# Kernel optimization log

Measured on AMD Instinct MI355X. Metric: run time of the kernel, lower is better.

The kernel has to match this reference:

```python
import jax, jax.numpy as jnp
import numpy as np

B, D, C = 4096, 4096, 1024


def setup_inputs() -> dict:
    key = jax.random.key(0)
    kx, kw = jax.random.split(key)
    x = jax.random.normal(kx, (B, D), dtype=jnp.float32)
    # kaiming_normal_ with nonlinearity='relu': std = sqrt(2 / fan_in)
    W = jax.random.normal(kw, (C, D), dtype=jnp.float32) * jnp.sqrt(2.0 / D)
    return {"x": x, "W": W}


def reference(x, W):
    # Original: -( (x[:, :, None] - W.T[None, :, :])**2 ).mean(axis=1)
    d = x.shape[1]
    x_sq = jnp.sum(x * x, axis=1, keepdims=True)        # [B, 1]
    w_sq = jnp.sum(W * W, axis=1)[None, :]              # [1, C]
    cross = jnp.einsum('bd,cd->bc', x, W)               # [B, C] tensor-core GEMM
    return -(x_sq - 2.0 * cross + w_sq) / d
```

## Files before the change

### kernel.cpp

```cpp
#include <hip/hip_runtime.h>
#include <hip/hip_bf16.h>


typedef float f32x4 __attribute__((ext_vector_type(4)));
typedef unsigned short ushort4_t __attribute__((ext_vector_type(4)));
typedef long long2_t __attribute__((ext_vector_type(2)));

#define BDIM 4096
#define DDIM 4096
#define CDIM 1024
#define TM 128
#define TN 128
#define BK 64
#define KSPLIT 4
#define NIT ((DDIM / KSPLIT) / BK)
#define SCALE 32.0f
#define INV_SS (1.0f/1024.0f)

__device__ __forceinline__ unsigned short f2bf(float f) {
    unsigned int u = __float_as_uint(f);
    unsigned int rounding = 0x7FFFu + ((u >> 16) & 1u);
    return (unsigned short)((u + rounding) >> 16);
}

__global__ __launch_bounds__(256) void cvt_rowsq(
    const float* __restrict__ x, const float* __restrict__ W,
    unsigned char* __restrict__ xb, unsigned char* __restrict__ wb,
    float* __restrict__ xsq, float* __restrict__ wsq)
{
    const int lane = threadIdx.x & 63;
    const int row = blockIdx.x * 4 + (threadIdx.x >> 6);

    const float* src;
    unsigned char* dst;
    float* sq;
    if (row < BDIM) {
        src = x + (size_t)row * DDIM;
        dst = xb + (size_t)row * DDIM;
        sq = xsq + row;
    } else {
        int r = row - BDIM;
        src = W + (size_t)r * DDIM;
        dst = wb + (size_t)r * DDIM;
        sq = wsq + r;
    }

    const float4* s4 = (const float4*)src;
    unsigned int* d4 = (unsigned int*)dst;
    float a = 0.f;
    #pragma unroll
    for (int s = 0; s < DDIM / 4 / 64; ++s) {
        float4 f = s4[lane + 64 * s];
        a += f.x * f.x + f.y * f.y + f.z * f.z + f.w * f.w;
        unsigned int p = 0;
        p = __builtin_amdgcn_cvt_pk_fp8_f32(f.x * SCALE, f.y * SCALE, p, false);
        p = __builtin_amdgcn_cvt_pk_fp8_f32(f.z * SCALE, f.w * SCALE, p, true);
        d4[lane + 64 * s] = p;
    }
    #pragma unroll
    for (int off = 32; off > 0; off >>= 1) a += __shfl_down(a, off);
    if (lane == 0) *sq = a;
}

__global__ __launch_bounds__(256, 3) void gemm_eucl(
    const unsigned char* __restrict__ xb,
    const unsigned char* __restrict__ wb,
    unsigned short* __restrict__ part)
{
    __shared__ unsigned char sm[2 * 16384];

    const int tid = threadIdx.x;
    const int lane = tid & 63;
    const int wid = tid >> 6;
    const int bm = blockIdx.x * TM;
    const int bn = blockIdx.y * TN;
    const int ks = blockIdx.z * (DDIM / KSPLIT);
    const int wm = (wid >> 1) * 64;
    const int wn = (wid & 1) * 64;

    const int r0 = tid >> 2, c = tid & 3;
    const unsigned char* gA0 = xb + (size_t)(bm + r0) * DDIM + ks + c * 16;
    const unsigned char* gA1 = gA0 + (size_t)64 * DDIM;
    const unsigned char* gB0 = wb + (size_t)(bn + r0) * DDIM + ks + c * 16;
    const unsigned char* gB1 = gB0 + (size_t)64 * DDIM;

    const int k2o = (c >> 1) * 8;
    const int kcw = (c & 1) * 2;
    const int wo0 = r0 * 64 + ((kcw ^ (r0 & 3)) * 16) + k2o;
    const int wo1 = r0 * 64 + (((kcw | 1) ^ (r0 & 3)) * 16) + k2o;

    const int kc = lane >> 4;
    const int ml = lane & 15;
    int aoff[4], boff[4];
    #pragma unroll
    for (int i = 0; i < 4; ++i) {
        int m = wm + i * 16 + ml;
        aoff[i] = m * 64 + ((kc ^ (m & 3)) * 16);
        int n = wn + i * 16 + ml;
        boff[i] = n * 64 + ((kc ^ (n & 3)) * 16);
    }

    f32x4 acc[4][4] = {};
    long2_t pA0, pA1, pB0, pB1;

    pA0 = *(const long2_t*)gA0; pA1 = *(const long2_t*)gA1;
    pB0 = *(const long2_t*)gB0; pB1 = *(const long2_t*)gB1;
    gA0 += BK; gA1 += BK; gB0 += BK; gB1 += BK;
    {
        unsigned char* sA = sm;
        unsigned char* sB = sm + 8192;
        *(long*)(sA + wo0) = pA0.x; *(long*)(sA + wo1) = pA0.y;
        *(long*)(sA + wo0 + 4096) = pA1.x; *(long*)(sA + wo1 + 4096) = pA1.y;
        *(long*)(sB + wo0) = pB0.x; *(long*)(sB + wo1) = pB0.y;
        *(long*)(sB + wo0 + 4096) = pB1.x; *(long*)(sB + wo1 + 4096) = pB1.y;
    }
    __syncthreads();

    int pb = 0;
    for (int k = 0; k < NIT - 1; ++k) {
        pA0 = *(const long2_t*)gA0; pA1 = *(const long2_t*)gA1;
        pB0 = *(const long2_t*)gB0; pB1 = *(const long2_t*)gB1;
        gA0 += BK; gA1 += BK; gB0 += BK; gB1 += BK;

        {
            const unsigned char* sA = sm + pb * 16384;
            const unsigned char* sB = sA + 8192;
            long2_t la[4], lb[4];
            #pragma unroll
            for (int i = 0; i < 4; ++i) la[i] = *(const long2_t*)(sA + aoff[i]);
            #pragma unroll
            for (int j = 0; j < 4; ++j) lb[j] = *(const long2_t*)(sB + boff[j]);
            #pragma unroll
            for (int i = 0; i < 4; ++i)
                #pragma unroll
                for (int j = 0; j < 4; ++j) {
                    acc[i][j] = __builtin_amdgcn_mfma_f32_16x16x32_fp8_fp8(
                        la[i].x, lb[j].x, acc[i][j], 0, 0, 0);
                    acc[i][j] = __builtin_amdgcn_mfma_f32_16x16x32_fp8_fp8(
                        la[i].y, lb[j].y, acc[i][j], 0, 0, 0);
                }
        }

        {
            unsigned char* sA = sm + (pb ^ 1) * 16384;
            unsigned char* sB = sA + 8192;
            *(long*)(sA + wo0) = pA0.x; *(long*)(sA + wo1) = pA0.y;
            *(long*)(sA + wo0 + 4096) = pA1.x; *(long*)(sA + wo1 + 4096) = pA1.y;
            *(long*)(sB + wo0) = pB0.x; *(long*)(sB + wo1) = pB0.y;
            *(long*)(sB + wo0 + 4096) = pB1.x; *(long*)(sB + wo1 + 4096) = pB1.y;
        }
        __syncthreads();
        pb ^= 1;
    }

    {
        const unsigned char* sA = sm + pb * 16384;
        const unsigned char* sB = sA + 8192;
        long2_t la[4], lb[4];
        #pragma unroll
        for (int i = 0; i < 4; ++i) la[i] = *(const long2_t*)(sA + aoff[i]);
        #pragma unroll
        for (int j = 0; j < 4; ++j) lb[j] = *(const long2_t*)(sB + boff[j]);
        #pragma unroll
        for (int i = 0; i < 4; ++i)
            #pragma unroll
            for (int j = 0; j < 4; ++j) {
                acc[i][j] = __builtin_amdgcn_mfma_f32_16x16x32_fp8_fp8(
                    la[i].x, lb[j].x, acc[i][j], 0, 0, 0);
                acc[i][j] = __builtin_amdgcn_mfma_f32_16x16x32_fp8_fp8(
                    la[i].y, lb[j].y, acc[i][j], 0, 0, 0);
            }
    }

    unsigned short* p = part + (size_t)blockIdx.z * BDIM * CDIM
                      + (size_t)(blockIdx.x * 8 + blockIdx.y) * 16384;
    #pragma unroll
    for (int i = 0; i < 4; ++i)
        #pragma unroll
        for (int j = 0; j < 4; ++j) {
            ushort4_t v;
            v[0] = f2bf(acc[i][j][0]); v[1] = f2bf(acc[i][j][1]);
            v[2] = f2bf(acc[i][j][2]); v[3] = f2bf(acc[i][j][3]);
            *(ushort4_t*)&p[(i * 4 + j) * 1024 + tid * 4] = v;
        }
}

__global__ __launch_bounds__(256) void reduce_out(
    const unsigned short* __restrict__ part, const float* __restrict__ xsq,
    const float* __restrict__ wsq, float* __restrict__ out)
{
    const int bb = blockIdx.x;
    const int t = threadIdx.x;
    const int lane = t & 63;
    const int wid = t >> 6;
    const int bm = (bb >> 3) * TM, bn = (bb & 7) * TN;
    const int wm = (wid >> 1) * 64, wn = (wid & 1) * 64;
    const int row_l = (lane >> 4) * 4, col_l = lane & 15;
    const size_t sl = (size_t)BDIM * CDIM;
    const float c1 = 2.0f * INV_SS / (float)DDIM;
    const float c2 = 1.0f / (float)DDIM;

    #pragma unroll
    for (int f = 0; f < 16; ++f) {
        size_t o = (size_t)bb * 16384 + f * 1024 + t * 4;
        ushort4_t p0 = *(const ushort4_t*)&part[o];
        ushort4_t p1 = *(const ushort4_t*)&part[o + sl];
        ushort4_t p2 = *(const ushort4_t*)&part[o + 2 * sl];
        ushort4_t p3 = *(const ushort4_t*)&part[o + 3 * sl];
        int i = f >> 2, j = f & 3;
        int gn = bn + wn + j * 16 + col_l;
        float wv = wsq[gn];
        #pragma unroll
        for (int r = 0; r < 4; ++r) {
            float s = __uint_as_float((unsigned int)p0[r] << 16)
                    + __uint_as_float((unsigned int)p1[r] << 16)
                    + __uint_as_float((unsigned int)p2[r] << 16)
                    + __uint_as_float((unsigned int)p3[r] << 16);
            int gm = bm + wm + i * 16 + row_l + r;
            out[(size_t)gm * CDIM + gn] = s * c1 - (xsq[gm] + wv) * c2;
        }
    }
}

__global__ void fallback_kernel(const float* __restrict__ x, const float* __restrict__ W,
                                float* __restrict__ out)
{
    int c = blockIdx.x * blockDim.x + threadIdx.x;
    int b = blockIdx.y;
    if (c >= CDIM) return;
    const float* xr = x + (size_t)b * DDIM;
    const float* wr = W + (size_t)c * DDIM;
    float xs = 0.f, ws = 0.f, cr = 0.f;
    for (int d = 0; d < DDIM; ++d) {
        float xv = xr[d], wv = wr[d];
        xs += xv * xv; ws += wv * wv; cr += xv * wv;
    }
    out[(size_t)b * CDIM + c] = (2.0f * cr - xs - ws) / (float)DDIM;
}

extern "C" void kernel_launch(void* const* d_in, const int* in_sizes, int n_in,
                              void* d_out, int out_size, void* d_ws, size_t ws_size,
                              hipStream_t stream) {
    const float* x = (const float*)d_in[0];
    const float* W = (const float*)d_in[1];
    float* out = (float*)d_out;

    size_t need = (size_t)(BDIM + CDIM) * DDIM
                + (size_t)(BDIM + CDIM) * sizeof(float)
                + (size_t)KSPLIT * BDIM * CDIM * 2;
    if (ws_size < need) {
        fallback_kernel<<<dim3(CDIM / 256, BDIM), 256, 0, stream>>>(x, W, out);
        return;
    }

    unsigned char* xb = (unsigned char*)d_ws;
    unsigned char* wb = xb + (size_t)BDIM * DDIM;
    float* xsq = (float*)(wb + (size_t)CDIM * DDIM);
    float* wsq = xsq + BDIM;
    unsigned short* part = (unsigned short*)(wsq + CDIM);

    cvt_rowsq<<<(BDIM + CDIM) / 4, 256, 0, stream>>>(x, W, xb, wb, xsq, wsq);
    gemm_eucl<<<dim3(BDIM / TM, CDIM / TN, KSPLIT), 256, 0, stream>>>(xb, wb, part);
    reduce_out<<<256, 256, 0, stream>>>(part, xsq, wsq, out);
}
```

Measured before the change: 149.9 us.

## Deepen global prefetch to two register sets and use an LDS-only barrier

The GEMM main loop now keeps two sets of global-load registers in flight, unrolled by two with explicit LDS buffer indices. It also swaps __syncthreads for an inline s_waitcnt lgkmcnt(0) plus s_barrier, so outstanding global loads no longer have to drain at every barrier. The goal is to hide more global-memory latency behind the MFMA work. The cost is extra VGPRs per thread, which could hurt occupancy under the 3-blocks-per-CU launch bound, and correctness now depends on the compiler placing vmcnt waits before the LDS writes.

```diff
diff --git a/kernel.cpp b/kernel.cpp
--- a/kernel.cpp
+++ b/kernel.cpp
@@ -16,6 +16,8 @@
 #define NIT ((DDIM / KSPLIT) / BK)
 #define SCALE 32.0f
 #define INV_SS (1.0f/1024.0f)
+
+#define SYNC_LGKM() asm volatile("s_waitcnt lgkmcnt(0)\n\ts_barrier" ::: "memory")
 
 __device__ __forceinline__ unsigned short f2bf(float f) {
     unsigned int u = __float_as_uint(f);
@@ -62,6 +64,8 @@
     if (lane == 0) *sq = a;
 }
 
+struct Pref { long2_t a0, a1, b0, b1; };
+
 __global__ __launch_bounds__(256, 3) void gemm_eucl(
     const unsigned char* __restrict__ xb,
     const unsigned char* __restrict__ wb,
@@ -101,76 +105,67 @@
     }
 
     f32x4 acc[4][4] = {};
-    long2_t pA0, pA1, pB0, pB1;
-
-    pA0 = *(const long2_t*)gA0; pA1 = *(const long2_t*)gA1;
-    pB0 = *(const long2_t*)gB0; pB1 = *(const long2_t*)gB1;
-    gA0 += BK; gA1 += BK; gB0 += BK; gB1 += BK;
-    {
-        unsigned char* sA = sm;
-        unsigned char* sB = sm + 8192;
-        *(long*)(sA + wo0) = pA0.x; *(long*)(sA + wo1) = pA0.y;
-        *(long*)(sA + wo0 + 4096) = pA1.x; *(long*)(sA + wo1 + 4096) = pA1.y;
-        *(long*)(sB + wo0) = pB0.x; *(long*)(sB + wo1) = pB0.y;
-        *(long*)(sB + wo0 + 4096) = pB1.x; *(long*)(sB + wo1 + 4096) = pB1.y;
-    }
-    __syncthreads();
-
-    int pb = 0;
-    for (int k = 0; k < NIT - 1; ++k) {
-        pA0 = *(const long2_t*)gA0; pA1 = *(const long2_t*)gA1;
-        pB0 = *(const long2_t*)gB0; pB1 = *(const long2_t*)gB1;
-        gA0 += BK; gA1 += BK; gB0 += BK; gB1 += BK;
-
-        {
-            const unsigned char* sA = sm + pb * 16384;
-            const unsigned char* sB = sA + 8192;
-            long2_t la[4], lb[4];
-            #pragma unroll
-            for (int i = 0; i < 4; ++i) la[i] = *(const long2_t*)(sA + aoff[i]);
-            #pragma unroll
-            for (int j = 0; j < 4; ++j) lb[j] = *(const long2_t*)(sB + boff[j]);
-            #pragma unroll
-            for (int i = 0; i < 4; ++i)
-                #pragma unroll
-                for (int j = 0; j < 4; ++j) {
-                    acc[i][j] = __builtin_amdgcn_mfma_f32_16x16x32_fp8_fp8(
-                        la[i].x, lb[j].x, acc[i][j], 0, 0, 0);
-                    acc[i][j] = __builtin_amdgcn_mfma_f32_16x16x32_fp8_fp8(
-                        la[i].y, lb[j].y, acc[i][j], 0, 0, 0);
-                }
-        }
-
-        {
-            unsigned char* sA = sm + (pb ^ 1) * 16384;
-            unsigned char* sB = sA + 8192;
-            *(long*)(sA + wo0) = pA0.x; *(long*)(sA + wo1) = pA0.y;
-            *(long*)(sA + wo0 + 4096) = pA1.x; *(long*)(sA + wo1 + 4096) = pA1.y;
-            *(long*)(sB + wo0) = pB0.x; *(long*)(sB + wo1) = pB0.y;
-            *(long*)(sB + wo0 + 4096) = pB1.x; *(long*)(sB + wo1 + 4096) = pB1.y;
-        }
-        __syncthreads();
-        pb ^= 1;
-    }
-
-    {
-        const unsigned char* sA = sm + pb * 16384;
-        const unsigned char* sB = sA + 8192;
-        long2_t la[4], lb[4];
-        #pragma unroll
-        for (int i = 0; i < 4; ++i) la[i] = *(const long2_t*)(sA + aoff[i]);
-        #pragma unroll
-        for (int j = 0; j < 4; ++j) lb[j] = *(const long2_t*)(sB + boff[j]);
-        #pragma unroll
-        for (int i = 0; i < 4; ++i)
-            #pragma unroll
-            for (int j = 0; j < 4; ++j) {
-                acc[i][j] = __builtin_amdgcn_mfma_f32_16x16x32_fp8_fp8(
-                    la[i].x, lb[j].x, acc[i][j], 0, 0, 0);
-                acc[i][j] = __builtin_amdgcn_mfma_f32_16x16x32_fp8_fp8(
-                    la[i].y, lb[j].y, acc[i][j], 0, 0, 0);
-            }
-    }
+
+#define LOADSET(S)                                                      \
+    do {                                                                \
+        (S).a0 = *(const long2_t*)gA0; (S).a1 = *(const long2_t*)gA1;   \
+        (S).b0 = *(const long2_t*)gB0; (S).b1 = *(const long2_t*)gB1;   \
+        gA0 += BK; gA1 += BK; gB0 += BK; gB1 += BK;                     \
+    } while (0)
+
+#define WRITESET(buf, S)                                                \
+    do {                                                                \
+        unsigned char* sA = sm + (buf) * 16384;                         \
+        unsigned char* sB = sA + 8192;                                  \
+        *(long*)(sA + wo0) = (S).a0.x; *(long*)(sA + wo1) = (S).a0.y;   \
+        *(long*)(sA + wo0 + 4096) = (S).a1.x;                           \
+        *(long*)(sA + wo1 + 4096) = (S).a1.y;                           \
+        *(long*)(sB + wo0) = (S).b0.x; *(long*)(sB + wo1) = (S).b0.y;   \
+        *(long*)(sB + wo0 + 4096) = (S).b1.x;                           \
+        *(long*)(sB + wo1 + 4096) = (S).b1.y;                           \
+    } while (0)
+
+#define COMPUTE(buf)                                                    \
+    do {                                                                \
+        const unsigned char* sA = sm + (buf) * 16384;                   \
+        const unsigned char* sB = sA + 8192;                            \
+        long2_t la[4], lb[4];                                           \
+        _Pragma("unroll")                                               \
+        for (int i = 0; i < 4; ++i) la[i] = *(const long2_t*)(sA + aoff[i]); \
+        _Pragma("unroll")                                               \
+        for (int j = 0; j < 4; ++j) lb[j] = *(const long2_t*)(sB + boff[j]); \
+        _Pragma("unroll")                                               \
+        for (int i = 0; i < 4; ++i)                                     \
+            _Pragma("unroll")                                           \
+            for (int j = 0; j < 4; ++j) {                               \
+                acc[i][j] = __builtin_amdgcn_mfma_f32_16x16x32_fp8_fp8( \
+                    la[i].x, lb[j].x, acc[i][j], 0, 0, 0);              \
+                acc[i][j] = __builtin_amdgcn_mfma_f32_16x16x32_fp8_fp8( \
+                    la[i].y, lb[j].y, acc[i][j], 0, 0, 0);              \
+            }                                                           \
+    } while (0)
+
+    Pref S0, S1;
+    LOADSET(S0);
+    LOADSET(S1);
+    WRITESET(0, S0);
+    SYNC_LGKM();
+
+    #pragma unroll 1
+    for (int kk = 0; kk < (NIT - 2) / 2; ++kk) {
+        LOADSET(S0);
+        COMPUTE(0);
+        WRITESET(1, S1);
+        SYNC_LGKM();
+        LOADSET(S1);
+        COMPUTE(1);
+        WRITESET(0, S0);
+        SYNC_LGKM();
+    }
+    COMPUTE(0);
+    WRITESET(1, S1);
+    SYNC_LGKM();
+    COMPUTE(1);
 
     unsigned short* p = part + (size_t)blockIdx.z * BDIM * CDIM
                       + (size_t)(blockIdx.x * 8 + blockIdx.y) * 16384;
@@ -183,6 +178,9 @@
             v[2] = f2bf(acc[i][j][2]); v[3] = f2bf(acc[i][j][3]);
             *(ushort4_t*)&p[(i * 4 + j) * 1024 + tid * 4] = v;
         }
+#undef LOADSET
+#undef WRITESET
+#undef COMPUTE
 }
 
 __global__ __launch_bounds__(256) void reduce_out(
```

Result: faster. 146.9 us (-2.0%).
